# Performance work log

Hardware: AMD Instinct MI355X
Metric: run time of the kernel (lower is better)

## Reference

```python
import jax, jax.numpy as jnp
import numpy as np

DIM = 256
DT_REF = 1.0
EPS = 1e-7
GATE_MIN, GATE_MAX = 0.01, 0.99


def _safe_forcing(exp_arg):
    # expm1(z)/z with denominator regularized by sign of real part (matches torch _safe_forcing)
    safe_denom = exp_arg + EPS * jnp.sign(exp_arg.real + EPS)
    return (jnp.exp(exp_arg) - 1.0) / safe_denom


def setup_inputs() -> dict:
    key = jax.random.key(0)
    ks = jax.random.split(key, 12)
    B, T, D = 8, 4096, DIM
    x_mean_seq = jax.random.normal(ks[0], (B, T, D), dtype=jnp.float32)
    dt_seq = jax.random.uniform(ks[1], (B, T), dtype=jnp.float32)
    # GlobalFluxTracker params
    decay_re = jax.random.normal(ks[2], (D,), dtype=jnp.float32) * 0.1 - 1.0
    decay_im = jax.random.normal(ks[3], (D,), dtype=jnp.float32) * 0.1
    W_in = jax.random.normal(ks[4], (2 * D, 2 * D), dtype=jnp.float32) * (1.0 / np.sqrt(2 * D))
    b_in = jnp.zeros((2 * D,), dtype=jnp.float32)
    W_out = jax.random.normal(ks[5], (2 * D, 2 * D), dtype=jnp.float32) * (1.0 / np.sqrt(2 * D))
    b_out = jnp.zeros((2 * D,), dtype=jnp.float32)
    W_gate = jax.random.normal(ks[6], (D, 2 * D), dtype=jnp.float32) * (1.0 / np.sqrt(2 * D))
    b_gate = jnp.zeros((D,), dtype=jnp.float32)
    # TemporalPropagator diagonal generator params
    lam_re = jax.random.normal(ks[7], (D,), dtype=jnp.float32) * 0.01
    lam_im = jax.random.normal(ks[8], (D,), dtype=jnp.float32) * 0.1
    return {
        "x_mean_seq": x_mean_seq, "dt_seq": dt_seq,
        "decay_re": decay_re, "decay_im": decay_im,
        "W_in": W_in, "b_in": b_in, "W_out": W_out, "b_out": b_out,
        "W_gate": W_gate, "b_gate": b_gate,
        "lam_re": lam_re, "lam_im": lam_im,
    }


def reference(x_mean_seq, dt_seq, decay_re, decay_im, W_in, b_in,
              W_out, b_out, W_gate, b_gate, lam_re, lam_im):
    # dt ratio [B,T,1]
    dt_ratio = (dt_seq / DT_REF)[..., None]

    # --- GlobalFluxTracker.get_scan_operators ---
    lam_f = -jax.nn.softplus(decay_re) + 1j * decay_im          # [D] complex64
    exp_arg = lam_f[None, None, :] * dt_ratio                    # [B,T,D]
    decay = jnp.exp(exp_arg)                                     # [B,T,D]
    forcing = _safe_forcing(exp_arg)                             # [B,T,D]

    # _mix_input on real input (imag part is zero)
    x_cat = jnp.concatenate([x_mean_seq, jnp.zeros_like(x_mean_seq)], axis=-1)
    x_in = x_cat @ W_in.T + b_in                                 # [B,T,2D]
    x_re, x_im = jnp.split(x_in, 2, axis=-1)
    x_mixed = x_re + 1j * x_im                                   # [B,T,D]
    X_scan = x_mixed * forcing                                   # [B,T,D]

    # --- linear recurrence flux_t = decay_t * flux_{t-1} + X_t (associative scan over T) ---
    def combine(c1, c2):
        a1, b1 = c1
        a2, b2 = c2
        return (a1 * a2, b1 * a2 + b2)
    _, flux = jax.lax.associative_scan(combine, (decay, X_scan), axis=1)  # [B,T,D]

    # --- compute_output_seq ---
    s_cat = jnp.concatenate([flux.real, flux.imag], axis=-1)     # [B,T,2D]
    src = s_cat @ W_out.T + b_out
    src_re, src_im = jnp.split(src, 2, axis=-1)
    gate = jax.nn.sigmoid(s_cat @ W_gate.T + b_gate)
    gate = gate * (GATE_MAX - GATE_MIN) + GATE_MIN               # [B,T,D]

    # --- TemporalPropagator.get_transition_operators_seq ---
    lam_p = -jax.nn.softplus(lam_re) + 1j * lam_im
    exp_arg_p = lam_p[None, None, :] * dt_ratio
    decay_p = jnp.exp(exp_arg_p)
    forcing_p = _safe_forcing(exp_arg_p)

    out = jnp.concatenate([
        src_re, src_im, gate,
        decay_p.real, decay_p.imag, forcing_p.real, forcing_p.imag,
    ], axis=-1)                                                  # [B,T,7D]
    return out
```

## Files before the change

### kernel.cpp

```cpp
#include <hip/hip_runtime.h>
#include <math.h>

#define DD 256
#define TT 4096
#define NBATCH 8
#define BTOK 32768
#define EPSF 1e-7f

typedef __attribute__((ext_vector_type(4))) float f32x4;
typedef __attribute__((ext_vector_type(8))) short bf16x8;

__device__ __forceinline__ float softplusf(float x) {
  float e = __expf(-fabsf(x));
  return fmaxf(x, 0.f) + __logf(1.f + e);
}
__device__ __forceinline__ float bf2f(unsigned short u) {
  union { unsigned int i; float f; } v; v.i = ((unsigned int)u) << 16; return v.f;
}
__device__ __forceinline__ unsigned short f2bf(float f) {
  union { float f; unsigned int i; } v; v.f = f;
  unsigned int x = v.i;
  unsigned int lsb = (x >> 16) & 1u;
  x += 0x7fffu + lsb;
  return (unsigned short)(x >> 16);
}
__device__ __forceinline__ void decay_forcing(float are, float aim,
    float& dre, float& dim, float& fre, float& fim) {
  float e = __expf(are);
  float s = __sinf(aim), c = __cosf(aim);
  dre = e * c; dim = e * s;
  float sg = (are + EPSF >= 0.f) ? 1.f : -1.f;
  float denr = are + EPSF * sg;
  float deni = aim;
  float inv = __builtin_amdgcn_rcpf(denr * denr + deni * deni);
  float nr = dre - 1.f, ni = dim;
  fre = (nr * denr + ni * deni) * inv;
  fim = (ni * denr - nr * deni) * inv;
}
__device__ __forceinline__ void gl_lds16(const void* g, void* l) {
  __builtin_amdgcn_global_load_lds(
      (const __attribute__((address_space(1))) unsigned int*)g,
      (__attribute__((address_space(3))) unsigned int*)l, 16, 0, 0);
}

__global__ __launch_bounds__(256) void prep(
    const float* __restrict__ x, unsigned short* __restrict__ Xb,
    const float* __restrict__ Win, unsigned short* __restrict__ Wp1,
    const float* __restrict__ Wout, const float* __restrict__ Wgate,
    unsigned short* __restrict__ Wp3)
{
  const int bid = blockIdx.x;
  if (bid < 8192) {
    size_t i = ((size_t)bid * 256 + threadIdx.x) * 4;
    float4 v = *reinterpret_cast<const float4*>(&x[i]);
    ushort4 u;
    u.x = f2bf(v.x); u.y = f2bf(v.y); u.z = f2bf(v.z); u.w = f2bf(v.w);
    *reinterpret_cast<ushort4*>(&Xb[i]) = u;
  } else if (bid < 8704) {
    const int p = bid - 8192;
    const int k = threadIdx.x;
    const int g = p >> 5, r = p & 31;
    const int src = (r < 16) ? (g * 16 + r) : (256 + g * 16 + (r - 16));
    Wp1[(size_t)p * 256 + k] = f2bf(Win[(size_t)src * 512 + k]);
  } else {
    const int p = bid - 8704;
    const float* src = (p < 512) ? (Wout + (size_t)p * 512)
                                 : (Wgate + (size_t)(p - 512) * 512);
    Wp3[(size_t)p * 512 + threadIdx.x] = f2bf(src[threadIdx.x]);
    Wp3[(size_t)p * 512 + threadIdx.x + 256] = f2bf(src[threadIdx.x + 256]);
  }
}

__global__ __launch_bounds__(256) void k1_mfma(
    const unsigned short* __restrict__ Xb,
    const unsigned short* __restrict__ Wp,
    const float* __restrict__ bin, const float* __restrict__ dts,
    const float* __restrict__ decr, const float* __restrict__ deci,
    unsigned short* __restrict__ Xre, unsigned short* __restrict__ Xim)
{
  __shared__ __align__(16) unsigned short As[128 * 64];
  __shared__ __align__(16) unsigned short Bs[128 * 64];
  const int bx = blockIdx.x;
  const int wg = (bx & 7) * 128 + (bx >> 3);
  const int mt = wg >> 2, nt = wg & 3;
  const int m0 = mt * 128, n0 = nt * 128;
  const int tid = threadIdx.x;
  const int lane = tid & 63, wid = tid >> 6;
  const int wr = wid >> 1, wc = wid & 1;
  const int l15 = lane & 15, hi = lane >> 4;
  const int lrow = tid >> 3;
  const int sslot = (tid & 7) ^ (lrow & 7);
  f32x4 acc[4][4];
  f32x4 z = {0.f, 0.f, 0.f, 0.f};
#pragma unroll
  for (int i = 0; i < 4; ++i)
#pragma unroll
    for (int j = 0; j < 4; ++j) acc[i][j] = z;

  for (int k0 = 0; k0 < 256; k0 += 64) {
    __syncthreads();
#pragma unroll
    for (int c = 0; c < 4; ++c) {
      gl_lds16(&Xb[(size_t)(m0 + c * 32 + lrow) * 256 + k0 + sslot * 8],
               &As[c * 2048 + tid * 8]);
      gl_lds16(&Wp[(size_t)(n0 + c * 32 + lrow) * 256 + k0 + sslot * 8],
               &Bs[c * 2048 + tid * 8]);
    }
    __syncthreads();
#pragma unroll
    for (int kk = 0; kk < 2; ++kk) {
      bf16x8 af[4], bfr[4];
      const int rslot = ((kk * 4 + hi) ^ (l15 & 7)) * 8;
#pragma unroll
      for (int m = 0; m < 4; ++m)
        af[m] = *reinterpret_cast<const bf16x8*>(&As[(wr * 64 + m * 16 + l15) * 64 + rslot]);
#pragma unroll
      for (int n = 0; n < 4; ++n)
        bfr[n] = *reinterpret_cast<const bf16x8*>(&Bs[(wc * 64 + n * 16 + l15) * 64 + rslot]);
#pragma unroll
      for (int m = 0; m < 4; ++m)
#pragma unroll
        for (int n = 0; n < 4; ++n)
          acc[m][n] = __builtin_amdgcn_mfma_f32_16x16x32_bf16(af[m], bfr[n], acc[m][n], 0, 0, 0);
    }
  }

  const int pbase = n0 + wc * 64;
#pragma unroll
  for (int pr = 0; pr < 2; ++pr) {
    const int d = (pbase >> 1) + pr * 16 + l15;
    const float nre = -softplusf(decr[d]);
    const float di = deci[d];
    const float br = bin[d], bi = bin[d + 256];
#pragma unroll
    for (int m = 0; m < 4; ++m) {
#pragma unroll
      for (int r = 0; r < 4; ++r) {
        const int row = m0 + wr * 64 + m * 16 + hi * 4 + r;
        float xr = acc[m][2 * pr][r] + br;
        float xi = acc[m][2 * pr + 1][r] + bi;
        float dt = dts[row];
        float are = nre * dt, aim = di * dt;
        float dr_, dm_, fr_, fm_;
        decay_forcing(are, aim, dr_, dm_, fr_, fm_);
        Xre[(size_t)row * DD + d] = f2bf(xr * fr_ - xi * fm_);
        Xim[(size_t)row * DD + d] = f2bf(xr * fm_ + xi * fr_);
      }
    }
  }
}

__global__ __launch_bounds__(256) void k2a_chunk(
    const unsigned short* __restrict__ Xre, const unsigned short* __restrict__ Xim,
    const float* __restrict__ dts, const float* __restrict__ decr, const float* __restrict__ deci,
    float4* __restrict__ ops)
{
  const int b = blockIdx.x >> 7;
  const int c = blockIdx.x & 127;
  const int d = threadIdx.x;
  __shared__ float sdt[32];
  if (threadIdx.x < 32) sdt[threadIdx.x] = dts[b * TT + c * 32 + threadIdx.x];
  float nre = -softplusf(decr[d]);
  float di = deci[d];
  __syncthreads();
  float Ar = 1.f, Ai = 0.f, Br2 = 0.f, Bi2 = 0.f;
  size_t base = (size_t)(b * TT + c * 32) * DD + d;
  for (int i = 0; i < 32; ++i) {
    float dt = sdt[i];
    float are = nre * dt, aim = di * dt;
    float e = __expf(are);
    float s = __sinf(aim), cs = __cosf(aim);
    float ar = e * cs, ai2 = e * s;
    float xr = bf2f(Xre[base]), xi = bf2f(Xim[base]);
    base += DD;
    float nAr = Ar * ar - Ai * ai2;
    float nAi = Ar * ai2 + Ai * ar;
    Ar = nAr; Ai = nAi;
    float nBr = Br2 * ar - Bi2 * ai2 + xr;
    float nBi = Br2 * ai2 + Bi2 * ar + xi;
    Br2 = nBr; Bi2 = nBi;
  }
  ops[(size_t)(b * 128 + c) * DD + d] = make_float4(Ar, Ai, Br2, Bi2);
}

__global__ __launch_bounds__(256) void k2b_carry(
    const float4* __restrict__ ops, float2* __restrict__ hin)
{
  const int b = blockIdx.x;
  const int d = threadIdx.x;
  float hr = 0.f, hi = 0.f;
  const size_t base = (size_t)b * 128 * DD + d;
  for (int c0 = 0; c0 < 128; c0 += 8) {
    float4 o0 = ops[base + (size_t)(c0 + 0) * DD];
    float4 o1 = ops[base + (size_t)(c0 + 1) * DD];
    float4 o2 = ops[base + (size_t)(c0 + 2) * DD];
    float4 o3 = ops[base + (size_t)(c0 + 3) * DD];
    float4 o4 = ops[base + (size_t)(c0 + 4) * DD];
    float4 o5 = ops[base + (size_t)(c0 + 5) * DD];
    float4 o6 = ops[base + (size_t)(c0 + 6) * DD];
    float4 o7 = ops[base + (size_t)(c0 + 7) * DD];
    float4 oo[8] = {o0, o1, o2, o3, o4, o5, o6, o7};
#pragma unroll
    for (int j = 0; j < 8; ++j) {
      hin[base + (size_t)(c0 + j) * DD] = make_float2(hr, hi);
      float nr = oo[j].x * hr - oo[j].y * hi + oo[j].z;
      float ni = oo[j].x * hi + oo[j].y * hr + oo[j].w;
      hr = nr; hi = ni;
    }
  }
}

__global__ __launch_bounds__(256) void k2c_apply(
    const unsigned short* __restrict__ Xre, const unsigned short* __restrict__ Xim,
    const float* __restrict__ dts, const float* __restrict__ decr, const float* __restrict__ deci,
    const float2* __restrict__ hin,
    unsigned short* __restrict__ F)
{
  const int b = blockIdx.x >> 7;
  const int c = blockIdx.x & 127;
  const int d = threadIdx.x;
  __shared__ float sdt[32];
  if (threadIdx.x < 32) sdt[threadIdx.x] = dts[b * TT + c * 32 + threadIdx.x];
  float nre = -softplusf(decr[d]);
  float di = deci[d];
  __syncthreads();
  float2 h = hin[(size_t)(b * 128 + c) * DD + d];
  float hr = h.x, hi = h.y;
  int tok = b * TT + c * 32;
  size_t base = (size_t)tok * DD + d;
  for (int i = 0; i < 32; ++i) {
    float dt = sdt[i];
    float are = nre * dt, aim = di * dt;
    float e = __expf(are);
    float s = __sinf(aim), cs = __cosf(aim);
    float ar = e * cs, ai2 = e * s;
    float xr = bf2f(Xre[base]), xi = bf2f(Xim[base]);
    float nr = ar * hr - ai2 * hi + xr;
    float ni = ar * hi + ai2 * hr + xi;
    hr = nr; hi = ni;
    size_t fb = (size_t)(tok + i) * 512 + d;
    F[fb] = f2bf(hr);
    F[fb + 256] = f2bf(hi);
    base += DD;
  }
}

__global__ __launch_bounds__(256) void k3k4(
    const unsigned short* __restrict__ F,
    const unsigned short* __restrict__ Wp,
    const float* __restrict__ bout, const float* __restrict__ bgate,
    const float* __restrict__ dts, const float* __restrict__ lre,
    const float* __restrict__ lim,
    float* __restrict__ out)
{
  __shared__ __align__(16) unsigned short As[128 * 64];
  __shared__ __align__(16) unsigned short Bs[128 * 64];

  if (blockIdx.x >= 1536) {
    const int pb = blockIdx.x - 1536;
    const int d = threadIdx.x;
    const float nl = -softplusf(lre[d]);
    const float li = lim[d];
    const int tok0 = pb * 32;
#pragma unroll 4
    for (int i = 0; i < 32; ++i) {
      const int tok = tok0 + i;
      float dt = dts[tok];
      float dr, dm, fr, fm;
      decay_forcing(nl * dt, li * dt, dr, dm, fr, fm);
      float* o = out + (size_t)tok * 1792 + 768;
      o[d] = dr; o[256 + d] = dm; o[512 + d] = fr; o[768 + d] = fm;
    }
    return;
  }

  const int bx = blockIdx.x;
  const int wg = (bx & 7) * 192 + (bx >> 3);
  const int mt = wg / 6, nt = wg % 6;
  const int m0 = mt * 128, n0 = nt * 128;
  const int tid = threadIdx.x;
  const int lane = tid & 63, wid = tid >> 6;
  const int wr = wid >> 1, wc = wid & 1;
  const int l15 = lane & 15, hi = lane >> 4;
  const int lrow = tid >> 3;
  const int sslot = (tid & 7) ^ (lrow & 7);
  f32x4 acc[4][4];
  f32x4 z = {0.f, 0.f, 0.f, 0.f};
#pragma unroll
  for (int i = 0; i < 4; ++i)
#pragma unroll
    for (int j = 0; j < 4; ++j) acc[i][j] = z;

  for (int k0 = 0; k0 < 512; k0 += 64) {
    __syncthreads();
#pragma unroll
    for (int c = 0; c < 4; ++c) {
      gl_lds16(&F[(size_t)(m0 + c * 32 + lrow) * 512 + k0 + sslot * 8],
               &As[c * 2048 + tid * 8]);
      gl_lds16(&Wp[(size_t)(n0 + c * 32 + lrow) * 512 + k0 + sslot * 8],
               &Bs[c * 2048 + tid * 8]);
    }
    __syncthreads();
#pragma unroll
    for (int kk = 0; kk < 2; ++kk) {
      bf16x8 af[4], bfr[4];
      const int rslot = ((kk * 4 + hi) ^ (l15 & 7)) * 8;
#pragma unroll
      for (int m = 0; m < 4; ++m)
        af[m] = *reinterpret_cast<const bf16x8*>(&As[(wr * 64 + m * 16 + l15) * 64 + rslot]);
#pragma unroll
      for (int n = 0; n < 4; ++n)
        bfr[n] = *reinterpret_cast<const bf16x8*>(&Bs[(wc * 64 + n * 16 + l15) * 64 + rslot]);
#pragma unroll
      for (int m = 0; m < 4; ++m)
#pragma unroll
        for (int n = 0; n < 4; ++n)
          acc[m][n] = __builtin_amdgcn_mfma_f32_16x16x32_bf16(af[m], bfr[n], acc[m][n], 0, 0, 0);
    }
  }

  const int nb = n0 + wc * 64;
  if (nb < 512) {
#pragma unroll
    for (int j = 0; j < 4; ++j) {
      const int col = nb + j * 16 + l15;
      const float bb = bout[col];
#pragma unroll
      for (int m = 0; m < 4; ++m)
#pragma unroll
        for (int r = 0; r < 4; ++r) {
          const int row = m0 + wr * 64 + m * 16 + hi * 4 + r;
          out[(size_t)row * 1792 + col] = acc[m][j][r] + bb;
        }
    }
  } else {
#pragma unroll
    for (int j = 0; j < 4; ++j) {
      const int col = nb + j * 16 + l15;
      const float bb = bgate[col - 512];
#pragma unroll
      for (int m = 0; m < 4; ++m)
#pragma unroll
        for (int r = 0; r < 4; ++r) {
          const int row = m0 + wr * 64 + m * 16 + hi * 4 + r;
          float g = __builtin_amdgcn_rcpf(1.f + __expf(-(acc[m][j][r] + bb)));
          out[(size_t)row * 1792 + col] = g * 0.98f + 0.01f;
        }
    }
  }
}

extern "C" void kernel_launch(void* const* d_in, const int* in_sizes, int n_in,
                              void* d_out, int out_size, void* d_ws, size_t ws_size,
                              hipStream_t stream)
{
  const float* x     = (const float*)d_in[0];
  const float* dts   = (const float*)d_in[1];
  const float* decr  = (const float*)d_in[2];
  const float* deci  = (const float*)d_in[3];
  const float* Win   = (const float*)d_in[4];
  const float* bin   = (const float*)d_in[5];
  const float* Wout  = (const float*)d_in[6];
  const float* bout  = (const float*)d_in[7];
  const float* Wgate = (const float*)d_in[8];
  const float* bgate = (const float*)d_in[9];
  const float* lre   = (const float*)d_in[10];
  const float* lim   = (const float*)d_in[11];
  float* out = (float*)d_out;
  char* ws = (char*)d_ws;

  unsigned short* F   = (unsigned short*)(ws);
  unsigned short* Xb  = (unsigned short*)(ws + (size_t)16 * 1024 * 1024);
  unsigned short* Xre = (unsigned short*)(ws + (size_t)32 * 1024 * 1024);
  unsigned short* Xim = (unsigned short*)(ws + (size_t)48 * 1024 * 1024);
  unsigned short* Wp1 = (unsigned short*)(ws + (size_t)64 * 1024 * 1024);
  unsigned short* Wp3 = (unsigned short*)(ws + (size_t)64 * 1024 * 1024 + 262144);
  float4* ops = (float4*)(ws + (size_t)65 * 1024 * 1024);
  float2* hin = (float2*)(ws + (size_t)69 * 1024 * 1024);

  prep<<<9472, 256, 0, stream>>>(x, Xb, Win, Wp1, Wout, Wgate, Wp3);
  k1_mfma<<<1024, 256, 0, stream>>>(Xb, Wp1, bin, dts, decr, deci, Xre, Xim);
  k2a_chunk<<<1024, 256, 0, stream>>>(Xre, Xim, dts, decr, deci, ops);
  k2b_carry<<<8, 256, 0, stream>>>(ops, hin);
  k2c_apply<<<1024, 256, 0, stream>>>(Xre, Xim, dts, decr, deci, hin, F);
  k3k4<<<2560, 256, 0, stream>>>(F, Wp3, bout, bgate, dts, lre, lim, out);
}
```

Measured before the change: 137.6 us.

## Fuse scan carry pass into apply kernel and pack real/imag scan inputs

Removes the separate 8-block carry-propagation kernel. Each apply block now redundantly folds the chunk operators of all preceding chunks to get its own initial state. Chunk length doubles from 32 to 64, halving the number of chunks, and the real and imaginary bf16 scan inputs are packed into one 32-bit word so each token needs a single load. This drops a serial low-occupancy launch and the hin round trip, at the cost of up to 63 redundant operator loads per block and only 512 blocks in the scan kernels.

```diff
diff --git a/kernel.cpp b/kernel.cpp
--- a/kernel.cpp
+++ b/kernel.cpp
@@ -76,7 +76,7 @@
     const unsigned short* __restrict__ Wp,
     const float* __restrict__ bin, const float* __restrict__ dts,
     const float* __restrict__ decr, const float* __restrict__ deci,
-    unsigned short* __restrict__ Xre, unsigned short* __restrict__ Xim)
+    unsigned int* __restrict__ Xri)
 {
   __shared__ __align__(16) unsigned short As[128 * 64];
   __shared__ __align__(16) unsigned short Bs[128 * 64];
@@ -143,105 +143,94 @@
         float are = nre * dt, aim = di * dt;
         float dr_, dm_, fr_, fm_;
         decay_forcing(are, aim, dr_, dm_, fr_, fm_);
-        Xre[(size_t)row * DD + d] = f2bf(xr * fr_ - xi * fm_);
-        Xim[(size_t)row * DD + d] = f2bf(xr * fm_ + xi * fr_);
+        unsigned int pk = (unsigned int)f2bf(xr * fr_ - xi * fm_)
+                        | ((unsigned int)f2bf(xr * fm_ + xi * fr_) << 16);
+        Xri[(size_t)row * DD + d] = pk;
       }
     }
   }
 }
 
 __global__ __launch_bounds__(256) void k2a_chunk(
-    const unsigned short* __restrict__ Xre, const unsigned short* __restrict__ Xim,
-    const float* __restrict__ dts, const float* __restrict__ decr, const float* __restrict__ deci,
+    const unsigned int* __restrict__ Xri,
+    const float* __restrict__ dts, const float* __restrict__ decr,
+    const float* __restrict__ deci,
     float4* __restrict__ ops)
 {
-  const int b = blockIdx.x >> 7;
-  const int c = blockIdx.x & 127;
+  const int bx = blockIdx.x;
+  const int b = bx >> 6, c = bx & 63;
   const int d = threadIdx.x;
-  __shared__ float sdt[32];
-  if (threadIdx.x < 32) sdt[threadIdx.x] = dts[b * TT + c * 32 + threadIdx.x];
-  float nre = -softplusf(decr[d]);
-  float di = deci[d];
+  __shared__ float sdt[64];
+  if (threadIdx.x < 64) sdt[threadIdx.x] = dts[b * TT + c * 64 + threadIdx.x];
+  const float nre = -softplusf(decr[d]);
+  const float di = deci[d];
   __syncthreads();
-  float Ar = 1.f, Ai = 0.f, Br2 = 0.f, Bi2 = 0.f;
-  size_t base = (size_t)(b * TT + c * 32) * DD + d;
-  for (int i = 0; i < 32; ++i) {
+  float Ar = 1.f, Ai = 0.f, Br = 0.f, Bi = 0.f;
+  size_t base = (size_t)(b * TT + c * 64) * DD + d;
+  for (int i = 0; i < 64; ++i) {
     float dt = sdt[i];
-    float are = nre * dt, aim = di * dt;
-    float e = __expf(are);
-    float s = __sinf(aim), cs = __cosf(aim);
-    float ar = e * cs, ai2 = e * s;
-    float xr = bf2f(Xre[base]), xi = bf2f(Xim[base]);
-    base += DD;
-    float nAr = Ar * ar - Ai * ai2;
-    float nAi = Ar * ai2 + Ai * ar;
+    float e = __expf(nre * dt);
+    float s = __sinf(di * dt), cs = __cosf(di * dt);
+    float ar = e * cs, ai = e * s;
+    unsigned int pk = Xri[base]; base += DD;
+    float xr = bf2f((unsigned short)(pk & 0xffffu));
+    float xi = bf2f((unsigned short)(pk >> 16));
+    float nAr = Ar * ar - Ai * ai, nAi = Ar * ai + Ai * ar;
     Ar = nAr; Ai = nAi;
-    float nBr = Br2 * ar - Bi2 * ai2 + xr;
-    float nBi = Br2 * ai2 + Bi2 * ar + xi;
-    Br2 = nBr; Bi2 = nBi;
-  }
-  ops[(size_t)(b * 128 + c) * DD + d] = make_float4(Ar, Ai, Br2, Bi2);
-}
-
-__global__ __launch_bounds__(256) void k2b_carry(
-    const float4* __restrict__ ops, float2* __restrict__ hin)
-{
-  const int b = blockIdx.x;
+    float nBr = Br * ar - Bi * ai + xr, nBi = Br * ai + Bi * ar + xi;
+    Br = nBr; Bi = nBi;
+  }
+  ops[(size_t)bx * DD + d] = make_float4(Ar, Ai, Br, Bi);
+}
+
+__global__ __launch_bounds__(256) void k2c_apply(
+    const unsigned int* __restrict__ Xri,
+    const float* __restrict__ dts, const float* __restrict__ decr,
+    const float* __restrict__ deci,
+    const float4* __restrict__ ops,
+    unsigned short* __restrict__ F)
+{
+  const int bx = blockIdx.x;
+  const int b = bx >> 6, c = bx & 63;
   const int d = threadIdx.x;
-  float hr = 0.f, hi = 0.f;
-  const size_t base = (size_t)b * 128 * DD + d;
-  for (int c0 = 0; c0 < 128; c0 += 8) {
-    float4 o0 = ops[base + (size_t)(c0 + 0) * DD];
-    float4 o1 = ops[base + (size_t)(c0 + 1) * DD];
-    float4 o2 = ops[base + (size_t)(c0 + 2) * DD];
-    float4 o3 = ops[base + (size_t)(c0 + 3) * DD];
-    float4 o4 = ops[base + (size_t)(c0 + 4) * DD];
-    float4 o5 = ops[base + (size_t)(c0 + 5) * DD];
-    float4 o6 = ops[base + (size_t)(c0 + 6) * DD];
-    float4 o7 = ops[base + (size_t)(c0 + 7) * DD];
-    float4 oo[8] = {o0, o1, o2, o3, o4, o5, o6, o7};
+  __shared__ float sdt[64];
+  if (threadIdx.x < 64) sdt[threadIdx.x] = dts[b * TT + c * 64 + threadIdx.x];
+  const float nre = -softplusf(decr[d]);
+  const float di = deci[d];
+  __syncthreads();
+
+  float hr = 0.f, hi2 = 0.f;
+  const size_t obase = (size_t)(b * 64) * DD + d;
+  for (int c0 = 0; c0 < c; c0 += 8) {
+    float4 oo[8];
+#pragma unroll
+    for (int j = 0; j < 8; ++j)
+      oo[j] = (c0 + j < c) ? ops[obase + (size_t)(c0 + j) * DD]
+                           : make_float4(1.f, 0.f, 0.f, 0.f);
 #pragma unroll
     for (int j = 0; j < 8; ++j) {
-      hin[base + (size_t)(c0 + j) * DD] = make_float2(hr, hi);
-      float nr = oo[j].x * hr - oo[j].y * hi + oo[j].z;
-      float ni = oo[j].x * hi + oo[j].y * hr + oo[j].w;
-      hr = nr; hi = ni;
-    }
-  }
-}
-
-__global__ __launch_bounds__(256) void k2c_apply(
-    const unsigned short* __restrict__ Xre, const unsigned short* __restrict__ Xim,
-    const float* __restrict__ dts, const float* __restrict__ decr, const float* __restrict__ deci,
-    const float2* __restrict__ hin,
-    unsigned short* __restrict__ F)
-{
-  const int b = blockIdx.x >> 7;
-  const int c = blockIdx.x & 127;
-  const int d = threadIdx.x;
-  __shared__ float sdt[32];
-  if (threadIdx.x < 32) sdt[threadIdx.x] = dts[b * TT + c * 32 + threadIdx.x];
-  float nre = -softplusf(decr[d]);
-  float di = deci[d];
-  __syncthreads();
-  float2 h = hin[(size_t)(b * 128 + c) * DD + d];
-  float hr = h.x, hi = h.y;
-  int tok = b * TT + c * 32;
-  size_t base = (size_t)tok * DD + d;
-  for (int i = 0; i < 32; ++i) {
+      float nr = oo[j].x * hr - oo[j].y * hi2 + oo[j].z;
+      float ni = oo[j].x * hi2 + oo[j].y * hr + oo[j].w;
+      hr = nr; hi2 = ni;
+    }
+  }
+
+  const int tok0 = b * TT + c * 64;
+  size_t base = (size_t)tok0 * DD + d;
+  for (int i = 0; i < 64; ++i) {
     float dt = sdt[i];
-    float are = nre * dt, aim = di * dt;
-    float e = __expf(are);
-    float s = __sinf(aim), cs = __cosf(aim);
-    float ar = e * cs, ai2 = e * s;
-    float xr = bf2f(Xre[base]), xi = bf2f(Xim[base]);
-    float nr = ar * hr - ai2 * hi + xr;
-    float ni = ar * hi + ai2 * hr + xi;
-    hr = nr; hi = ni;
-    size_t fb = (size_t)(tok + i) * 512 + d;
+    float e = __expf(nre * dt);
+    float s = __sinf(di * dt), cs = __cosf(di * dt);
+    float ar = e * cs, ai = e * s;
+    unsigned int pk = Xri[base]; base += DD;
+    float xr = bf2f((unsigned short)(pk & 0xffffu));
+    float xi = bf2f((unsigned short)(pk >> 16));
+    float nr = ar * hr - ai * hi2 + xr;
+    float ni = ar * hi2 + ai * hr + xi;
+    hr = nr; hi2 = ni;
+    size_t fb = (size_t)(tok0 + i) * 512 + d;
     F[fb] = f2bf(hr);
-    F[fb + 256] = f2bf(hi);
-    base += DD;
+    F[fb + 256] = f2bf(hi2);
   }
 }
 
@@ -371,17 +360,14 @@
 
   unsigned short* F   = (unsigned short*)(ws);
   unsigned short* Xb  = (unsigned short*)(ws + (size_t)16 * 1024 * 1024);
-  unsigned short* Xre = (unsigned short*)(ws + (size_t)32 * 1024 * 1024);
-  unsigned short* Xim = (unsigned short*)(ws + (size_t)48 * 1024 * 1024);
+  unsigned int*  Xri  = (unsigned int*)(ws + (size_t)32 * 1024 * 1024);
   unsigned short* Wp1 = (unsigned short*)(ws + (size_t)64 * 1024 * 1024);
   unsigned short* Wp3 = (unsigned short*)(ws + (size_t)64 * 1024 * 1024 + 262144);
   float4* ops = (float4*)(ws + (size_t)65 * 1024 * 1024);
-  float2* hin = (float2*)(ws + (size_t)69 * 1024 * 1024);
 
   prep<<<9472, 256, 0, stream>>>(x, Xb, Win, Wp1, Wout, Wgate, Wp3);
-  k1_mfma<<<1024, 256, 0, stream>>>(Xb, Wp1, bin, dts, decr, deci, Xre, Xim);
-  k2a_chunk<<<1024, 256, 0, stream>>>(Xre, Xim, dts, decr, deci, ops);
-  k2b_carry<<<8, 256, 0, stream>>>(ops, hin);
-  k2c_apply<<<1024, 256, 0, stream>>>(Xre, Xim, dts, decr, deci, hin, F);
+  k1_mfma<<<1024, 256, 0, stream>>>(Xb, Wp1, bin, dts, decr, deci, Xri);
+  k2a_chunk<<<512, 256, 0, stream>>>(Xri, dts, decr, deci, ops);
+  k2c_apply<<<512, 256, 0, stream>>>(Xri, dts, decr, deci, ops, F);
   k3k4<<<2560, 256, 0, stream>>>(F, Wp3, bout, bgate, dts, lre, lim, out);
 }
```

Result: no change. 136.1 us (-1.1%).
